# Performance work log

Hardware: AMD Instinct MI355X
Metric: run time of the kernel (lower is better)

## Reference

```python
import jax, jax.numpy as jnp
import numpy as np
from jax.scipy.special import erfc

CUTOFF = 10.0   # real-space cutoff (Angstrom)
ALPHA = 0.3     # Ewald splitting parameter (1/Angstrom)
KMAX = 8        # max integer k-index per dimension
N_ATOMS = 4096
BOX = 40.0      # cubic box edge (Angstrom)


def setup_inputs() -> dict:
    key = jax.random.key(0)
    kp, kq = jax.random.split(key)
    positions = jax.random.uniform(kp, (N_ATOMS, 3), dtype=jnp.float32) * BOX
    charges = jax.random.normal(kq, (N_ATOMS,), dtype=jnp.float32)
    charges = charges - charges.mean()  # enforce charge neutrality
    cell = jnp.eye(3, dtype=jnp.float32) * BOX  # row-vector lattice
    return {"positions": positions, "charges": charges, "cell": cell}


def _kvectors(kmax):
    # static integer grid (-kmax..kmax)^3 \\ {0}, built with numpy at trace time
    n = np.arange(-kmax, kmax + 1)
    grid = np.stack(np.meshgrid(n, n, n, indexing="ij"), axis=-1).reshape(-1, 3)
    grid = grid[np.any(grid != 0, axis=-1)]
    return jnp.asarray(grid, dtype=jnp.float32)  # [Nk, 3]


def _ewald(positions, charges, cell, cutoff, alpha, kmax):
    N = positions.shape[0]
    inv_cell = jnp.linalg.inv(cell)

    # ---- real-space sum: 0.5 * sum_{i!=j, r<rc} q_i q_j erfc(a r)/r (min image)
    rij = positions[:, None, :] - positions[None, :, :]          # [N,N,3]
    frac = rij @ inv_cell
    rij = (frac - jnp.round(frac)) @ cell                        # minimum image
    r2 = jnp.sum(rij * rij, axis=-1)                             # [N,N]
    eye = jnp.eye(N, dtype=bool)
    r = jnp.sqrt(jnp.where(eye, 1.0, r2))                        # safe sqrt on diag
    pair_mask = (~eye) & (r2 < cutoff * cutoff)
    qq = charges[:, None] * charges[None, :]
    e_real = 0.5 * jnp.sum(jnp.where(pair_mask, qq * erfc(alpha * r) / r, 0.0))

    # ---- reciprocal-space sum: (2pi/V) sum_k exp(-k^2/4a^2)/k^2 |S(k)|^2
    recip = 2.0 * jnp.pi * inv_cell.T                            # reciprocal lattice rows
    kvecs = _kvectors(kmax) @ recip                              # [Nk,3]
    k2 = jnp.sum(kvecs * kvecs, axis=-1)                         # [Nk]
    phase = positions @ kvecs.T                                  # [N,Nk]
    s_re = charges @ jnp.cos(phase)                              # [Nk]
    s_im = charges @ jnp.sin(phase)                              # [Nk]
    vol = jnp.abs(jnp.linalg.det(cell))
    coeff = jnp.exp(-k2 / (4.0 * alpha * alpha)) / k2
    e_recip = (2.0 * jnp.pi / vol) * jnp.sum(coeff * (s_re * s_re + s_im * s_im))

    # ---- self-energy correction
    e_self = -(alpha / jnp.sqrt(jnp.pi)) * jnp.sum(charges * charges)

    return e_real + e_recip + e_self


def reference(positions, charges, cell):
    return _ewald(positions, charges, cell, CUTOFF, ALPHA, KMAX)
```

## Files before the change

### kernel.cpp

```cpp
#include <hip/hip_runtime.h>
#include <math.h>

#define ALPHA 0.3f
#define KMAX 8
#define KDIM 17
#define KD2 (KDIM*KDIM)
#define NK_FULL (KDIM*KDIM*KDIM - 1)
#define NK_HALF (NK_FULL/2)
#define RECIP_KPB 16
#define NB_RECIP ((NK_HALF + RECIP_KPB - 1)/RECIP_KPB)
#define TWO_PI 6.28318530717958647692f

#define SELF_COEF (-0.16925687506432687f)
#define INV_4A2 (1.0f/(4.0f*ALPHA*ALPHA))
#define C1A (0.3275911f*ALPHA)
#define NA2 (-(ALPHA*ALPHA))
#define B1 0.0835179f
#define B2 0.02073501f
#define B3 2.624400e-5f
#define B4 6.326748e-4f

#define ITILE 256
#define JTILE 128

__device__ __forceinline__ void invert3x3(const float* __restrict__ c, float inv[9], float* det_out) {
    float a00=c[0],a01=c[1],a02=c[2];
    float a10=c[3],a11=c[4],a12=c[5];
    float a20=c[6],a21=c[7],a22=c[8];
    float c00 =  a11*a22 - a12*a21;
    float c01 = -(a10*a22 - a12*a20);
    float c02 =  a10*a21 - a11*a20;
    float det = a00*c00 + a01*c01 + a02*c02;
    float id = 1.0f/det;
    inv[0] =  c00*id;
    inv[1] = -(a01*a22 - a02*a21)*id;
    inv[2] =  (a01*a12 - a02*a11)*id;
    inv[3] =  c01*id;
    inv[4] =  (a00*a22 - a02*a20)*id;
    inv[5] = -(a00*a12 - a02*a10)*id;
    inv[6] =  c02*id;
    inv[7] = -(a00*a21 - a01*a20)*id;
    inv[8] =  (a00*a11 - a01*a10)*id;
    *det_out = det;
}

__device__ __forceinline__ float erfc_a(float r, float r2) {
    float t = __builtin_amdgcn_rcpf(fmaf(C1A, r, 1.0f));
    float p = t * fmaf(t, fmaf(t, fmaf(t, fmaf(t, 1.061405429f, -1.453152027f),
                       1.421413741f), -0.284496736f), 0.254829592f);
    return p * __expf(NA2 * r2);
}

__device__ __forceinline__ float pair_ortho(float4 p, float xi, float yi, float zi,
                                            float i0, float i4, float i8,
                                            float c0, float c4, float c8) {
    float dx = xi - p.x, dy = yi - p.y, dz = zi - p.z;
    float rx = fmaf(-c0, rintf(dx * i0), dx);
    float ry = fmaf(-c4, rintf(dy * i4), dy);
    float rz = fmaf(-c8, rintf(dz * i8), dz);
    float r2 = fmaf(rx, rx, fmaf(ry, ry, rz * rz));
    float rinv = __builtin_amdgcn_rsqf(r2);
    float r = r2 * rinv;
    float pl = fmaf(r, fmaf(r, fmaf(r, fmaf(r, B4, B3), B2), B1), 1.0f);
    float y  = __builtin_amdgcn_rsqf(pl);
    float y2 = y * y;
    float y4 = y2 * y2;
    float y8 = y4 * y4;
    return p.w * rinv * y8;
}

__device__ __forceinline__ float block_reduce(float v) {
    for (int o = 32; o > 0; o >>= 1) v += __shfl_down(v, o, 64);
    __shared__ float smem[4];
    int lane = threadIdx.x & 63, wid = threadIdx.x >> 6;
    if (lane == 0) smem[wid] = v;
    __syncthreads();
    int nw = blockDim.x >> 6;
    v = ((int)threadIdx.x < nw) ? smem[threadIdx.x] : 0.0f;
    if (wid == 0) {
        for (int o = 4; o > 0; o >>= 1) v += __shfl_down(v, o, 64);
    }
    return v;
}

__global__ __launch_bounds__(256) void fused_kernel(const float* __restrict__ pos,
                                                    const float* __restrict__ q,
                                                    const float* __restrict__ cell,
                                                    float* __restrict__ e_out,
                                                    int N, int nb_recip, int nb_real) {
    __shared__ float4 rtile[256];
    __shared__ float red[128][33];
    __shared__ float red2[8][33];
    float inv[9]; float det;
    invert3x3(cell, inv, &det);
    bool ortho = (cell[1]==0.f) & (cell[2]==0.f) & (cell[3]==0.f) &
                 (cell[5]==0.f) & (cell[6]==0.f) & (cell[7]==0.f);

    int bid = blockIdx.x;
    int tid = threadIdx.x;
    int lane = tid & 63, wid = tid >> 6;

    if (bid < nb_recip) {
        int kbase = bid * RECIP_KPB;
        int m = kbase % KDIM;
        int wj = (16 - m) % KDIM;
        bool kxw = ((kbase + wj) % KD2) == (KD2 - 1);
        int wj_s  = __builtin_amdgcn_readfirstlane(wj);
        int kxw_s = __builtin_amdgcn_readfirstlane((int)kxw);
        float fkx0 = (float)(kbase / KD2 - KMAX);
        float fky0 = (float)((kbase / KDIM) % KDIM - KMAX);
        float fkz0 = (float)(kbase % KDIM - KMAX);

        float ar[RECIP_KPB], ai[RECIP_KPB];
        #pragma unroll
        for (int j = 0; j < RECIP_KPB; ++j) { ar[j] = 0.0f; ai[j] = 0.0f; }

        int nrounds = (N + 255) >> 8;
        for (int r = 0; r < nrounds; ++r) {
            int a = (r << 8) + tid;
            if (a < N) {
                float x = pos[3*a], y = pos[3*a+1], z = pos[3*a+2];
                float qa = q[a];
                float wx, wy, wz;
                if (ortho) { wx = x*inv[0]; wy = y*inv[4]; wz = z*inv[8]; }
                else {
                    wx = inv[0]*x + inv[3]*y + inv[6]*z;
                    wy = inv[1]*x + inv[4]*y + inv[7]*z;
                    wz = inv[2]*x + inv[5]*y + inv[8]*z;
                }
                float ph0 = fmaf(fkx0, wx, fmaf(fky0, wy, fkz0 * wz));
                ph0 -= rintf(ph0);
                float az = wz - rintf(wz);
                float aw = kxw_s ? (wx - 16.0f*wy - 17.0f*wz)
                                 : (wy - 17.0f*wz);
                aw -= rintf(aw);
                float c0 = __builtin_amdgcn_cosf(ph0), s0 = __builtin_amdgcn_sinf(ph0);
                float zc = __builtin_amdgcn_cosf(az),  zs = __builtin_amdgcn_sinf(az);
                float wc = __builtin_amdgcn_cosf(aw),  ws = __builtin_amdgcn_sinf(aw);
                float pr = qa * c0, pi = qa * s0;
                #pragma unroll
                for (int j = 0; j < RECIP_KPB; ++j) {
                    ar[j] += pr; ai[j] += pi;
                    if (j < RECIP_KPB - 1) {
                        float nr = pr*zc - pi*zs;
                        float ni = pr*zs + pi*zc;
                        pr = nr; pi = ni;
                        if (j == wj_s) {
                            nr = pr*wc - pi*ws;
                            ni = pr*ws + pi*wc;
                            pr = nr; pi = ni;
                        }
                    }
                }
            }
        }

        #pragma unroll
        for (int j = 0; j < RECIP_KPB; ++j) {
            ar[j] += __shfl_down(ar[j], 32, 64);
            ai[j] += __shfl_down(ai[j], 32, 64);
        }
        if (lane < 32) {
            int row = (wid << 5) | lane;
            #pragma unroll
            for (int j = 0; j < RECIP_KPB; ++j) {
                red[row][j]             = ar[j];
                red[row][RECIP_KPB + j] = ai[j];
            }
        }
        __syncthreads();
        {
            int v = tid & 31, grp = tid >> 5;
            float s = 0.0f;
            int r0 = grp << 4;
            #pragma unroll 4
            for (int rr = 0; rr < 16; ++rr) s += red[r0 + rr][v];
            red2[grp][v] = s;
        }
        __syncthreads();
        if (tid < 32) {
            float tot = 0.0f;
            #pragma unroll
            for (int g = 0; g < 8; ++g) tot += red2[g][tid];
            float other = __shfl_down(tot, 16, 64);
            float e = 0.0f;
            if (tid < 16) {
                int t = kbase + tid;
                if (t < NK_HALF) {
                    float nx = (float)(t / KD2 - KMAX);
                    float ny = (float)((t / KDIM) % KDIM - KMAX);
                    float nz = (float)(t % KDIM - KMAX);
                    float kvx = TWO_PI * (nx*inv[0] + ny*inv[1] + nz*inv[2]);
                    float kvy = TWO_PI * (nx*inv[3] + ny*inv[4] + nz*inv[5]);
                    float kvz = TWO_PI * (nx*inv[6] + ny*inv[7] + nz*inv[8]);
                    float k2 = fmaf(kvx, kvx, fmaf(kvy, kvy, kvz * kvz));
                    float vol = fabsf(det);
                    float pref = 2.0f * (TWO_PI / vol);
                    float coeff = __expf(-k2 * INV_4A2) * __builtin_amdgcn_rcpf(k2);
                    e = pref * coeff * fmaf(tot, tot, other * other);
                }
                for (int o = 8; o > 0; o >>= 1) e += __shfl_down(e, o, 64);
                if (tid == 0) unsafeAtomicAdd(e_out, e);
            }
        }
        if (bid == nb_recip - 1) {
            float fa = 0.0f;
            for (int t = tid; t < N; t += 256) {
                float qt = q[t];
                fa = fmaf(SELF_COEF * qt, qt, fa);
            }
            __syncthreads();
            float s2 = block_reduce(fa);
            if (tid == 0) unsafeAtomicAdd(e_out, s2);
        }
    } else {
        int rbid = bid - nb_recip;
        int bi = 0, acc = 0;
        for (;;) {
            int up = min(N, (bi + 1) * ITILE);
            int nc = (up + JTILE - 1) / JTILE;
            if (rbid < acc + nc) break;
            acc += nc; ++bi;
        }
        int bj = rbid - acc;

        float c0 = cell[0], c4 = cell[4], c8 = cell[8];
        float c1 = cell[1], c2 = cell[2], c3 = cell[3];
        float c5 = cell[5], c6 = cell[6], c7 = cell[7];

        int ibase = bi * ITILE;
        int i = ibase + tid;
        bool ivalid = (i < N);
        float xi = 0.f, yi = 0.f, zi = 0.f, qi = 0.f;
        if (ivalid) { xi = pos[3*i]; yi = pos[3*i+1]; zi = pos[3*i+2]; qi = q[i]; }

        int jbase = bj * JTILE;
        int jcount = min(JTILE, N - jbase);
        if (tid < jcount) {
            int j = jbase + tid;
            rtile[tid] = make_float4(pos[3*j], pos[3*j+1], pos[3*j+2], q[j]);
        }
        __syncthreads();

        bool full = (jbase + JTILE <= ibase) && (ibase + ITILE <= N) && (jcount == JTILE);

        float e0 = 0.0f, e1 = 0.0f, e2 = 0.0f, e3 = 0.0f;
        if (ortho) {
            float i0 = inv[0], i4 = inv[4], i8 = inv[8];
            if (full) {
                #pragma unroll 2
                for (int t = 0; t < JTILE; t += 4) {
                    float4 p0 = rtile[t+0], p1 = rtile[t+1], p2 = rtile[t+2], p3 = rtile[t+3];
                    e0 += pair_ortho(p0, xi, yi, zi, i0, i4, i8, c0, c4, c8);
                    e1 += pair_ortho(p1, xi, yi, zi, i0, i4, i8, c0, c4, c8);
                    e2 += pair_ortho(p2, xi, yi, zi, i0, i4, i8, c0, c4, c8);
                    e3 += pair_ortho(p3, xi, yi, zi, i0, i4, i8, c0, c4, c8);
                }
            } else {
                int t = 0;
                for (; t + 3 < jcount; t += 4) {
                    float4 p0 = rtile[t+0], p1 = rtile[t+1], p2 = rtile[t+2], p3 = rtile[t+3];
                    float v0 = pair_ortho(p0, xi, yi, zi, i0, i4, i8, c0, c4, c8);
                    float v1 = pair_ortho(p1, xi, yi, zi, i0, i4, i8, c0, c4, c8);
                    float v2 = pair_ortho(p2, xi, yi, zi, i0, i4, i8, c0, c4, c8);
                    float v3 = pair_ortho(p3, xi, yi, zi, i0, i4, i8, c0, c4, c8);
                    bool k0 = ivalid && ((jbase + t + 0) < i);
                    bool k1 = ivalid && ((jbase + t + 1) < i);
                    bool k2 = ivalid && ((jbase + t + 2) < i);
                    bool k3 = ivalid && ((jbase + t + 3) < i);
                    e0 += k0 ? v0 : 0.0f;
                    e1 += k1 ? v1 : 0.0f;
                    e2 += k2 ? v2 : 0.0f;
                    e3 += k3 ? v3 : 0.0f;
                }
                for (; t < jcount; ++t) {
                    float4 p = rtile[t];
                    float v = pair_ortho(p, xi, yi, zi, i0, i4, i8, c0, c4, c8);
                    bool ok = ivalid && ((jbase + t) < i);
                    e0 += ok ? v : 0.0f;
                }
            }
        } else {
            for (int t = 0; t < jcount; ++t) {
                float4 p = rtile[t];
                float dx = xi - p.x, dy = yi - p.y, dz = zi - p.z;
                float fx = dx*inv[0] + dy*inv[3] + dz*inv[6];
                float fy = dx*inv[1] + dy*inv[4] + dz*inv[7];
                float fz = dx*inv[2] + dy*inv[5] + dz*inv[8];
                fx -= rintf(fx); fy -= rintf(fy); fz -= rintf(fz);
                float rx = fx*c0 + fy*c3 + fz*c6;
                float ry = fx*c1 + fy*c4 + fz*c7;
                float rz = fx*c2 + fy*c5 + fz*c8;
                float r2 = fmaf(rx, rx, fmaf(ry, ry, rz * rz));
                float rinv = __builtin_amdgcn_rsqf(r2);
                float r = r2 * rinv;
                float val = p.w * rinv * erfc_a(r, r2);
                bool ok = ivalid && ((jbase + t) < i);
                e0 += ok ? val : 0.0f;
            }
        }
        float acc_e = ((e0 + e1) + (e2 + e3)) * qi;

        float s = block_reduce(acc_e);
        if (tid == 0) unsafeAtomicAdd(e_out, s);
    }
}

extern "C" void kernel_launch(void* const* d_in, const int* in_sizes, int n_in,
                              void* d_out, int out_size, void* d_ws, size_t ws_size,
                              hipStream_t stream) {
    const float* pos  = (const float*)d_in[0];
    const float* q    = (const float*)d_in[1];
    const float* cell = (const float*)d_in[2];
    int N = in_sizes[1];
    float* e_out = (float*)d_out;

    int nbi = (N + ITILE - 1) / ITILE;
    int nb_real = 0;
    for (int bi = 0; bi < nbi; ++bi) {
        int up = (N < (bi + 1) * ITILE) ? N : (bi + 1) * ITILE;
        nb_real += (up + JTILE - 1) / JTILE;
    }
    int nb_recip = NB_RECIP;

    hipMemsetAsync(e_out, 0, sizeof(float), stream);

    fused_kernel<<<nb_recip + nb_real, 256, 0, stream>>>(pos, q, cell, e_out,
                                                         N, nb_recip, nb_real);
}
```

Measured before the change: 73.73 us.

## Spatially bin atoms in a pre-pass and skip real-space tiles beyond cutoff

```diff
diff --git a/kernel.cpp b/kernel.cpp
--- a/kernel.cpp
+++ b/kernel.cpp
@@ -10,6 +10,7 @@
 #define RECIP_KPB 16
 #define NB_RECIP ((NK_HALF + RECIP_KPB - 1)/RECIP_KPB)
 #define TWO_PI 6.28318530717958647692f
+#define RC2 100.0f
 
 #define SELF_COEF (-0.16925687506432687f)
 #define INV_4A2 (1.0f/(4.0f*ALPHA*ALPHA))
@@ -83,8 +84,101 @@
     return v;
 }
 
-__global__ __launch_bounds__(256) void fused_kernel(const float* __restrict__ pos,
+__device__ __forceinline__ void block_minmax3(float mn[3], float mx[3]) {
+    __shared__ float sm[4][8];
+    int lane = threadIdx.x & 63, wid = threadIdx.x >> 6;
+    #pragma unroll
+    for (int d = 0; d < 3; ++d) {
+        float a = mn[d], b = mx[d];
+        for (int o = 32; o > 0; o >>= 1) {
+            a = fminf(a, __shfl_down(a, o, 64));
+            b = fmaxf(b, __shfl_down(b, o, 64));
+        }
+        if (lane == 0) { sm[wid][d] = a; sm[wid][4 + d] = b; }
+    }
+    __syncthreads();
+    #pragma unroll
+    for (int d = 0; d < 3; ++d) {
+        float a = fminf(fminf(sm[0][d], sm[1][d]), fminf(sm[2][d], sm[3][d]));
+        float b = fmaxf(fmaxf(sm[0][4+d], sm[1][4+d]), fmaxf(sm[2][4+d], sm[3][4+d]));
+        mn[d] = a; mx[d] = b;
+    }
+    __syncthreads();
+}
+
+__global__ __launch_bounds__(1024) void sort_kernel(const float* __restrict__ pos,
                                                     const float* __restrict__ q,
+                                                    const float* __restrict__ cell,
+                                                    float4* __restrict__ sorted,
+                                                    float* __restrict__ e_out,
+                                                    int N) {
+    __shared__ unsigned hist[64];
+    __shared__ unsigned offs[64];
+    __shared__ float smem[16];
+    float inv[9]; float det;
+    invert3x3(cell, inv, &det);
+    bool ortho = (cell[1]==0.f) & (cell[2]==0.f) & (cell[3]==0.f) &
+                 (cell[5]==0.f) & (cell[6]==0.f) & (cell[7]==0.f);
+    int tid = threadIdx.x;
+    if (tid < 64) hist[tid] = 0u;
+    __syncthreads();
+
+    int nrounds = (N + 1023) >> 10;
+    for (int r = 0; r < nrounds; ++r) {
+        int a = (r << 10) + tid;
+        if (a < N) {
+            float x = pos[3*a], y = pos[3*a+1], z = pos[3*a+2];
+            float wx, wy, wz;
+            if (ortho) { wx = x*inv[0]; wy = y*inv[4]; wz = z*inv[8]; }
+            else {
+                wx = inv[0]*x + inv[3]*y + inv[6]*z;
+                wy = inv[1]*x + inv[4]*y + inv[7]*z;
+                wz = inv[2]*x + inv[5]*y + inv[8]*z;
+            }
+            wx -= floorf(wx); wy -= floorf(wy); wz -= floorf(wz);
+            int cx = min(3, (int)(wx*4.0f)), cy = min(3, (int)(wy*4.0f)), cz = min(3, (int)(wz*4.0f));
+            atomicAdd(&hist[(cx<<4)|(cy<<2)|cz], 1u);
+        }
+    }
+    __syncthreads();
+    if (tid == 0) {
+        unsigned s = 0;
+        for (int i = 0; i < 64; ++i) { offs[i] = s; s += hist[i]; }
+    }
+    __syncthreads();
+
+    float fa = 0.0f;
+    for (int r = 0; r < nrounds; ++r) {
+        int a = (r << 10) + tid;
+        if (a < N) {
+            float x = pos[3*a], y = pos[3*a+1], z = pos[3*a+2];
+            float qa = q[a];
+            float wx, wy, wz;
+            if (ortho) { wx = x*inv[0]; wy = y*inv[4]; wz = z*inv[8]; }
+            else {
+                wx = inv[0]*x + inv[3]*y + inv[6]*z;
+                wy = inv[1]*x + inv[4]*y + inv[7]*z;
+                wz = inv[2]*x + inv[5]*y + inv[8]*z;
+            }
+            wx -= floorf(wx); wy -= floorf(wy); wz -= floorf(wz);
+            int cx = min(3, (int)(wx*4.0f)), cy = min(3, (int)(wy*4.0f)), cz = min(3, (int)(wz*4.0f));
+            unsigned rank = atomicAdd(&offs[(cx<<4)|(cy<<2)|cz], 1u);
+            sorted[rank] = make_float4(x, y, z, qa);
+            fa = fmaf(SELF_COEF * qa, qa, fa);
+        }
+    }
+    for (int o = 32; o > 0; o >>= 1) fa += __shfl_down(fa, o, 64);
+    int lane = tid & 63, wid = tid >> 6;
+    if (lane == 0) smem[wid] = fa;
+    __syncthreads();
+    if (wid == 0) {
+        float v = (lane < 16) ? smem[lane] : 0.0f;
+        for (int o = 8; o > 0; o >>= 1) v += __shfl_down(v, o, 64);
+        if (lane == 0) e_out[0] = v;
+    }
+}
+
+__global__ __launch_bounds__(256) void fused_kernel(const float4* __restrict__ sorted,
                                                     const float* __restrict__ cell,
                                                     float* __restrict__ e_out,
                                                     int N, int nb_recip, int nb_real) {
@@ -119,14 +213,14 @@
         for (int r = 0; r < nrounds; ++r) {
             int a = (r << 8) + tid;
             if (a < N) {
-                float x = pos[3*a], y = pos[3*a+1], z = pos[3*a+2];
-                float qa = q[a];
+                float4 s4 = sorted[a];
+                float qa = s4.w;
                 float wx, wy, wz;
-                if (ortho) { wx = x*inv[0]; wy = y*inv[4]; wz = z*inv[8]; }
+                if (ortho) { wx = s4.x*inv[0]; wy = s4.y*inv[4]; wz = s4.z*inv[8]; }
                 else {
-                    wx = inv[0]*x + inv[3]*y + inv[6]*z;
-                    wy = inv[1]*x + inv[4]*y + inv[7]*z;
-                    wz = inv[2]*x + inv[5]*y + inv[8]*z;
+                    wx = inv[0]*s4.x + inv[3]*s4.y + inv[6]*s4.z;
+                    wy = inv[1]*s4.x + inv[4]*s4.y + inv[7]*s4.z;
+                    wz = inv[2]*s4.x + inv[5]*s4.y + inv[8]*s4.z;
                 }
                 float ph0 = fmaf(fkx0, wx, fmaf(fky0, wy, fkz0 * wz));
                 ph0 -= rintf(ph0);
@@ -203,16 +297,6 @@
                 if (tid == 0) unsafeAtomicAdd(e_out, e);
             }
         }
-        if (bid == nb_recip - 1) {
-            float fa = 0.0f;
-            for (int t = tid; t < N; t += 256) {
-                float qt = q[t];
-                fa = fmaf(SELF_COEF * qt, qt, fa);
-            }
-            __syncthreads();
-            float s2 = block_reduce(fa);
-            if (tid == 0) unsafeAtomicAdd(e_out, s2);
-        }
     } else {
         int rbid = bid - nb_recip;
         int bi = 0, acc = 0;
@@ -232,77 +316,109 @@
         int i = ibase + tid;
         bool ivalid = (i < N);
         float xi = 0.f, yi = 0.f, zi = 0.f, qi = 0.f;
-        if (ivalid) { xi = pos[3*i]; yi = pos[3*i+1]; zi = pos[3*i+2]; qi = q[i]; }
+        if (ivalid) { float4 p4 = sorted[i]; xi = p4.x; yi = p4.y; zi = p4.z; qi = p4.w; }
 
         int jbase = bj * JTILE;
         int jcount = min(JTILE, N - jbase);
-        if (tid < jcount) {
-            int j = jbase + tid;
-            rtile[tid] = make_float4(pos[3*j], pos[3*j+1], pos[3*j+2], q[j]);
+        float jx = 0.f, jy = 0.f, jz = 0.f;
+        bool jloader = (tid < jcount);
+        if (jloader) {
+            float4 p4 = sorted[jbase + tid];
+            rtile[tid] = p4;
+            jx = p4.x; jy = p4.y; jz = p4.z;
         }
         __syncthreads();
 
+        bool skip = false;
+        if (ortho) {
+            float mn[3], mx[3];
+            mn[0] = ivalid ? xi :  1e30f;  mx[0] = ivalid ? xi : -1e30f;
+            mn[1] = ivalid ? yi :  1e30f;  mx[1] = ivalid ? yi : -1e30f;
+            mn[2] = ivalid ? zi :  1e30f;  mx[2] = ivalid ? zi : -1e30f;
+            block_minmax3(mn, mx);
+            float imn[3] = {mn[0], mn[1], mn[2]}, imx[3] = {mx[0], mx[1], mx[2]};
+            mn[0] = jloader ? jx :  1e30f;  mx[0] = jloader ? jx : -1e30f;
+            mn[1] = jloader ? jy :  1e30f;  mx[1] = jloader ? jy : -1e30f;
+            mn[2] = jloader ? jz :  1e30f;  mx[2] = jloader ? jz : -1e30f;
+            block_minmax3(mn, mx);
+            float L[3]  = {c0, c4, c8};
+            float iL[3] = {inv[0], inv[4], inv[8]};
+            float g2 = 0.0f;
+            #pragma unroll
+            for (int d = 0; d < 3; ++d) {
+                float ci = 0.5f*(imn[d] + imx[d]), wi = imx[d] - imn[d];
+                float cj = 0.5f*(mn[d] + mx[d]),  wjd = mx[d] - mn[d];
+                float dc = ci - cj;
+                dc -= L[d] * rintf(dc * iL[d]);
+                float g = fmaxf(0.0f, fabsf(dc) - 0.5f*(wi + wjd));
+                g2 = fmaf(g, g, g2);
+            }
+            skip = (g2 >= RC2);
+        }
+
         bool full = (jbase + JTILE <= ibase) && (ibase + ITILE <= N) && (jcount == JTILE);
 
         float e0 = 0.0f, e1 = 0.0f, e2 = 0.0f, e3 = 0.0f;
-        if (ortho) {
-            float i0 = inv[0], i4 = inv[4], i8 = inv[8];
-            if (full) {
-                #pragma unroll 2
-                for (int t = 0; t < JTILE; t += 4) {
-                    float4 p0 = rtile[t+0], p1 = rtile[t+1], p2 = rtile[t+2], p3 = rtile[t+3];
-                    e0 += pair_ortho(p0, xi, yi, zi, i0, i4, i8, c0, c4, c8);
-                    e1 += pair_ortho(p1, xi, yi, zi, i0, i4, i8, c0, c4, c8);
-                    e2 += pair_ortho(p2, xi, yi, zi, i0, i4, i8, c0, c4, c8);
-                    e3 += pair_ortho(p3, xi, yi, zi, i0, i4, i8, c0, c4, c8);
+        if (!skip) {
+            if (ortho) {
+                float i0 = inv[0], i4 = inv[4], i8 = inv[8];
+                if (full) {
+                    #pragma unroll 2
+                    for (int t = 0; t < JTILE; t += 4) {
+                        float4 p0 = rtile[t+0], p1 = rtile[t+1], p2 = rtile[t+2], p3 = rtile[t+3];
+                        e0 += pair_ortho(p0, xi, yi, zi, i0, i4, i8, c0, c4, c8);
+                        e1 += pair_ortho(p1, xi, yi, zi, i0, i4, i8, c0, c4, c8);
+                        e2 += pair_ortho(p2, xi, yi, zi, i0, i4, i8, c0, c4, c8);
+                        e3 += pair_ortho(p3, xi, yi, zi, i0, i4, i8, c0, c4, c8);
+                    }
+                } else {
+                    int t = 0;
+                    for (; t + 3 < jcount; t += 4) {
+                        float4 p0 = rtile[t+0], p1 = rtile[t+1], p2 = rtile[t+2], p3 = rtile[t+3];
+                        float v0 = pair_ortho(p0, xi, yi, zi, i0, i4, i8, c0, c4, c8);
+                        float v1 = pair_ortho(p1, xi, yi, zi, i0, i4, i8, c0, c4, c8);
+                        float v2 = pair_ortho(p2, xi, yi, zi, i0, i4, i8, c0, c4, c8);
+                        float v3 = pair_ortho(p3, xi, yi, zi, i0, i4, i8, c0, c4, c8);
+                        bool k0 = ivalid && ((jbase + t + 0) < i);
+                        bool k1 = ivalid && ((jbase + t + 1) < i);
+                        bool k2 = ivalid && ((jbase + t + 2) < i);
+                        bool k3 = ivalid && ((jbase + t + 3) < i);
+                        e0 += k0 ? v0 : 0.0f;
+                        e1 += k1 ? v1 : 0.0f;
+                        e2 += k2 ? v2 : 0.0f;
+                        e3 += k3 ? v3 : 0.0f;
+                    }
+                    for (; t < jcount; ++t) {
+                        float4 p = rtile[t];
+                        float v = pair_ortho(p, xi, yi, zi, i0, i4, i8, c0, c4, c8);
+                        bool ok = ivalid && ((jbase + t) < i);
+                        e0 += ok ? v : 0.0f;
+                    }
                 }
             } else {
-                int t = 0;
-                for (; t + 3 < jcount; t += 4) {
-                    float4 p0 = rtile[t+0], p1 = rtile[t+1], p2 = rtile[t+2], p3 = rtile[t+3];
-                    float v0 = pair_ortho(p0, xi, yi, zi, i0, i4, i8, c0, c4, c8);
-                    float v1 = pair_ortho(p1, xi, yi, zi, i0, i4, i8, c0, c4, c8);
-                    float v2 = pair_ortho(p2, xi, yi, zi, i0, i4, i8, c0, c4, c8);
-                    float v3 = pair_ortho(p3, xi, yi, zi, i0, i4, i8, c0, c4, c8);
-                    bool k0 = ivalid && ((jbase + t + 0) < i);
-                    bool k1 = ivalid && ((jbase + t + 1) < i);
-                    bool k2 = ivalid && ((jbase + t + 2) < i);
-                    bool k3 = ivalid && ((jbase + t + 3) < i);
-                    e0 += k0 ? v0 : 0.0f;
-                    e1 += k1 ? v1 : 0.0f;
-                    e2 += k2 ? v2 : 0.0f;
-                    e3 += k3 ? v3 : 0.0f;
+                for (int t = 0; t < jcount; ++t) {
+                    float4 p = rtile[t];
+                    float dx = xi - p.x, dy = yi - p.y, dz = zi - p.z;
+                    float fx = dx*inv[0] + dy*inv[3] + dz*inv[6];
+                    float fy = dx*inv[1] + dy*inv[4] + dz*inv[7];
+                    float fz = dx*inv[2] + dy*inv[5] + dz*inv[8];
+                    fx -= rintf(fx); fy -= rintf(fy); fz -= rintf(fz);
+                    float rx = fx*c0 + fy*c3 + fz*c6;
+                    float ry = fx*c1 + fy*c4 + fz*c7;
+                    float rz = fx*c2 + fy*c5 + fz*c8;
+                    float r2 = fmaf(rx, rx, fmaf(ry, ry, rz * rz));
+                    float rinv = __builtin_amdgcn_rsqf(r2);
+                    float r = r2 * rinv;
+                    float val = p.w * rinv * erfc_a(r, r2);
+                    bool ok = ivalid && ((jbase + t) < i);
+                    e0 += ok ? val : 0.0f;
                 }
-                for (; t < jcount; ++t) {
-                    float4 p = rtile[t];
-                    float v = pair_ortho(p, xi, yi, zi, i0, i4, i8, c0, c4, c8);
-                    bool ok = ivalid && ((jbase + t) < i);
-                    e0 += ok ? v : 0.0f;
-                }
-            }
-        } else {
-            for (int t = 0; t < jcount; ++t) {
-                float4 p = rtile[t];
-                float dx = xi - p.x, dy = yi - p.y, dz = zi - p.z;
-                float fx = dx*inv[0] + dy*inv[3] + dz*inv[6];
-                float fy = dx*inv[1] + dy*inv[4] + dz*inv[7];
-                float fz = dx*inv[2] + dy*inv[5] + dz*inv[8];
-                fx -= rintf(fx); fy -= rintf(fy); fz -= rintf(fz);
-                float rx = fx*c0 + fy*c3 + fz*c6;
-                float ry = fx*c1 + fy*c4 + fz*c7;
-                float rz = fx*c2 + fy*c5 + fz*c8;
-                float r2 = fmaf(rx, rx, fmaf(ry, ry, rz * rz));
-                float rinv = __builtin_amdgcn_rsqf(r2);
-                float r = r2 * rinv;
-                float val = p.w * rinv * erfc_a(r, r2);
-                bool ok = ivalid && ((jbase + t) < i);
-                e0 += ok ? val : 0.0f;
             }
         }
         float acc_e = ((e0 + e1) + (e2 + e3)) * qi;
 
         float s = block_reduce(acc_e);
-        if (tid == 0) unsafeAtomicAdd(e_out, s);
+        if (tid == 0 && s != 0.0f) unsafeAtomicAdd(e_out, s);
     }
 }
 
@@ -314,6 +430,7 @@
     const float* cell = (const float*)d_in[2];
     int N = in_sizes[1];
     float* e_out = (float*)d_out;
+    float4* sorted = (float4*)d_ws;
 
     int nbi = (N + ITILE - 1) / ITILE;
     int nb_real = 0;
@@ -323,8 +440,8 @@
     }
     int nb_recip = NB_RECIP;
 
-    hipMemsetAsync(e_out, 0, sizeof(float), stream);
-
-    fused_kernel<<<nb_recip + nb_real, 256, 0, stream>>>(pos, q, cell, e_out,
+    sort_kernel<<<1, 1024, 0, stream>>>(pos, q, cell, sorted, e_out, N);
+
+    fused_kernel<<<nb_recip + nb_real, 256, 0, stream>>>(sorted, cell, e_out,
                                                          N, nb_recip, nb_real);
 }
```

Result: slower. 81.93 us (+11.1%).
